# Kernel optimization log

Measured on AMD Instinct MI355X. Metric: run time of the kernel, lower is better.

## Reference

```python
import jax, jax.numpy as jnp
import numpy as np

X_DIM = 20000   # number of input locations (x_l rows)
Y_DIM = 6000    # number of query locations (y_l rows)
REGION_DEG = 10.0  # lon/lat spread so every query has neighbors within 250 km
EARTH_DIAM = 2.0 * 6.378  # thousand-km diameter used by the source
THRESH = 0.25   # 250 km neighborhood threshold


def setup_inputs() -> dict:
    key = jax.random.key(0)
    k1, k2, k3 = jax.random.split(key, 3)
    x = jax.random.normal(k1, (X_DIM, 1), dtype=jnp.float32)
    x_l = jax.random.uniform(k2, (X_DIM, 2), dtype=jnp.float32) * REGION_DEG
    y_l = jax.random.uniform(k3, (Y_DIM, 2), dtype=jnp.float32) * REGION_DEG
    return {"x": x, "x_l": x_l, "y_l": y_l}


def reference(x, x_l, y_l):
    # Training branch of GPR.call, vectorized over the y_dim python loop.
    d2r = jnp.pi / 180.0
    lon_x, lat_x = x_l[:, 0], x_l[:, 1]   # (X,)
    lon_y, lat_y = y_l[:, 0], y_l[:, 1]   # (Y,)
    # haversine terms, shape (Y, X)
    hav = jnp.sin((lat_x[None, :] - lat_y[:, None]) * d2r) ** 2
    hav = hav + (jnp.cos(lat_x * d2r)[None, :] * jnp.cos(lat_y * d2r)[:, None]
                 * jnp.sin((lon_x[None, :] - lon_y[:, None]) * d2r) ** 2)
    d = EARTH_DIAM * jnp.arcsin(jnp.sqrt(hav))  # great-circle distance (thousand km)
    # threshold + gather/scatter in source == masked weights here
    w = jnp.where(d < THRESH, d, 0.0)
    s = jnp.sum(w, axis=1, keepdims=True)        # (Y, 1) per-row normalizer
    L = jnp.where(s > 0, w / jnp.maximum(s, 1e-12), 0.0)  # (Y, X) sparse-ish weights
    m = (L @ x)[:, 0]                            # (Y,) squeezed mean
    # V = 0.001 * I  (noise=None path); returned value is diag_part(V)
    v_diag = jnp.full((y_l.shape[0],), 0.001, dtype=x.dtype)
    return m, v_diag
```

## Files before the change

### kernel.cpp

```cpp
#include <hip/hip_runtime.h>
#include <math.h>


#define TPB    256
#define NSTRIP 40
#define NLON   40
#define NCELLS (NSTRIP * NLON)
#define C_CELL   0.25f
#define INV_CELL 4.0f
#define RLAT     1.1250f

__device__ __forceinline__ float sin_poly(float a) {
    float t = a * a;
    return a * fmaf(t, fmaf(t, 8.3333333e-3f, -0.16666667f), 1.0f);
}
__device__ __forceinline__ float cos_poly(float a) {
    float t = a * a;
    return fmaf(t, fmaf(t, fmaf(t, -1.3888889e-3f, 4.1666668e-2f), -0.5f), 1.0f);
}
__device__ __forceinline__ int cell_of(float lon, float lat) {
    int s = (int)(lat * INV_CELL); s = min(max(s, 0), NSTRIP - 1);
    int l = (int)(lon * INV_CELL); l = min(max(l, 0), NLON - 1);
    return s * NLON + l;
}

__device__ __attribute__((noinline)) float band_w(float lonx, float latx,
                                                  float lony, float laty)
{
    const float d2r = 0.017453292519943295f;
    float dlat = __fsub_rn(latx, laty);
    float alat = __fmul_rn(dlat, d2r);
    float slf  = (float)sin((double)alat);
    float h1   = __fmul_rn(slf, slf);

    float axl  = __fmul_rn(latx, d2r);
    float ayl  = __fmul_rn(laty, d2r);
    float cxf  = (float)cos((double)axl);
    float cyf  = (float)cos((double)ayl);
    float cc   = __fmul_rn(cxf, cyf);

    float dlon = __fsub_rn(lonx, lony);
    float alon = __fmul_rn(dlon, d2r);
    float sdf  = (float)sin((double)alon);
    float h2   = __fmul_rn(sdf, sdf);

    float hv   = __fadd_rn(h1, __fmul_rn(cc, h2));
    float r32  = (float)sqrt((double)hv);
    float as32 = (float)asin((double)r32);
    float dnp  = __fmul_rn(12.756f, as32);
    return (dnp < 0.25f) ? dnp : 0.0f;
}


__global__ __launch_bounds__(TPB) void zero_kernel(int* __restrict__ histX,
                                                   int* __restrict__ histY) {
    for (int i = threadIdx.x; i < NCELLS; i += TPB) { histX[i] = 0; histY[i] = 0; }
}

__global__ __launch_bounds__(TPB) void hist_kernel(
    const float* __restrict__ x_l, const float* __restrict__ y_l,
    int* __restrict__ histX, int* __restrict__ histY, int nx, int ny)
{
    int i = blockIdx.x * TPB + threadIdx.x;
    if (i < nx) {
        atomicAdd(&histX[cell_of(x_l[2 * i], x_l[2 * i + 1])], 1);
    } else if (i < nx + ny) {
        int j = i - nx;
        atomicAdd(&histY[cell_of(y_l[2 * j], y_l[2 * j + 1])], 1);
    }
}

__global__ __launch_bounds__(TPB) void scan_kernel(
    const int* __restrict__ histX, const int* __restrict__ histY,
    int* __restrict__ csX, int* __restrict__ csY,
    int* __restrict__ curX, int* __restrict__ curY)
{
    const int CHUNK = (NCELLS + TPB - 1) / TPB;
    __shared__ int sums[TPB];
    const int* hist      = (blockIdx.x == 0) ? histX : histY;
    int*       cellStart = (blockIdx.x == 0) ? csX  : csY;
    int*       cursor    = (blockIdx.x == 0) ? curX : curY;

    int tid = threadIdx.x;
    int base = tid * CHUNK;
    int local[7];
    int s = 0;
    #pragma unroll
    for (int j = 0; j < CHUNK; ++j) {
        int idx = base + j;
        int v = (idx < NCELLS) ? hist[idx] : 0;
        local[j] = s; s += v;
    }
    sums[tid] = s;
    __syncthreads();
    for (int off = 1; off < TPB; off <<= 1) {
        int t = (tid >= off) ? sums[tid - off] : 0;
        __syncthreads();
        sums[tid] += t;
        __syncthreads();
    }
    int excl = (tid > 0) ? sums[tid - 1] : 0;
    #pragma unroll
    for (int j = 0; j < CHUNK; ++j) {
        int idx = base + j;
        if (idx < NCELLS) { cellStart[idx] = excl + local[j]; cursor[idx] = excl + local[j]; }
    }
    if (tid == TPB - 1) cellStart[NCELLS] = sums[TPB - 1];
}

__global__ __launch_bounds__(TPB) void scatter_kernel(
    const float* __restrict__ x, const float* __restrict__ x_l,
    const float* __restrict__ y_l,
    int* __restrict__ curX, int* __restrict__ curY,
    float4* __restrict__ sortedA, float2* __restrict__ sortedRaw,
    float2* __restrict__ sortedYL, int* __restrict__ sortedYIdx,
    int nx, int ny)
{
    const float d2r = 0.017453292519943295f;
    int i = blockIdx.x * TPB + threadIdx.x;
    if (i < nx) {
        float lon = x_l[2 * i], lat = x_l[2 * i + 1];
        int pos = atomicAdd(&curX[cell_of(lon, lat)], 1);
        float al = lat * d2r, ao = lon * d2r;
        sortedA[pos]   = make_float4(sin_poly(al), sin_poly(ao),
                                     cos_poly(ao), x[i]);
        sortedRaw[pos] = make_float2(lon, lat);
    } else if (i < nx + ny) {
        int j = i - nx;
        float lon = y_l[2 * j], lat = y_l[2 * j + 1];
        int pos = atomicAdd(&curY[cell_of(lon, lat)], 1);
        sortedYL[pos]   = make_float2(lon, lat);
        sortedYIdx[pos] = j;
    }
}


__global__ __launch_bounds__(TPB) void gpr_binned(
    const float4* __restrict__ sortedA,
    const float2* __restrict__ sortedRaw,
    const int*    __restrict__ cellStart,
    const float2* __restrict__ sortedYL,
    const int*    __restrict__ sortedYIdx,
    float* __restrict__ out, int ny, float Hcut, float HcutM)
{
    const int tid  = threadIdx.x;
    const int wave = tid >> 6;
    const int lane = tid & 63;
    const int wid  = blockIdx.x * (TPB / 64) + wave;
    const int j0   = 2 * wid;
    const int j1   = j0 + 1;
    if (j0 >= ny) return;
    const bool has1 = (j1 < ny);

    const float d2r    = 0.017453292519943295f;
    const float r2d    = 57.29577951308232f;
    const float DIAM   = 12.756f;
    const float DIAM6  = 12.756f / 6.0f;
    const float EPS_H  = 5e-8f;

    const int    yi0 = sortedYIdx[j0];
    const float2 q0  = sortedYL[j0];
    const int    yi1 = has1 ? sortedYIdx[j1] : yi0;
    const float2 q1  = has1 ? sortedYL[j1] : q0;

    const float lon0 = q0.x, lat0 = q0.y;
    const float lon1 = q1.x, lat1 = q1.y;

    const float sly0 = sin_poly(lat0 * d2r), cly0 = cos_poly(lat0 * d2r);
    const float slo0 = sin_poly(lon0 * d2r), clo0 = cos_poly(lon0 * d2r);
    const float sly1 = sin_poly(lat1 * d2r), cly1 = cos_poly(lat1 * d2r);
    const float slo1 = sin_poly(lon1 * d2r), clo1 = cos_poly(lon1 * d2r);

    float accw0 = 0.0f, accx0 = 0.0f, accw1 = 0.0f, accx1 = 0.0f;

    const float latmin = fminf(lat0, lat1), latmax = fmaxf(lat0, lat1);
    const int s0 = max(0,          (int)floorf((latmin - RLAT) * INV_CELL));
    const int s1 = min(NSTRIP - 1, (int)floorf((latmax + RLAT) * INV_CELL));

    for (int s = s0; s <= s1; ++s) {
        const float slo = s * C_CELL, shi = slo + C_CELL;
        const float ccs = cos_poly(fminf(shi, 10.0f) * d2r) * 0.999999f;

        int lo = NLON, hi = -1;
        {
            float dmin = fmaxf(0.0f, fmaxf(slo - lat0, lat0 - shi));
            float de   = fmaxf(0.0f, dmin - 3e-3f);
            float sp   = sin_poly(de * d2r);
            float rem  = HcutM - sp * sp;
            if (rem > 0.0f) {
                float rr = __builtin_amdgcn_sqrtf(rem / (ccs * cly0));
                float W  = rr * fmaf(rr * rr, 0.16666667f, 1.0f) * r2d + 4e-3f;
                lo = min(lo, min(NLON - 1, max(0, (int)floorf((lon0 - W) * INV_CELL))));
                hi = max(hi, min(NLON - 1, max(0, (int)floorf((lon0 + W) * INV_CELL))));
            }
        }
        {
            float dmin = fmaxf(0.0f, fmaxf(slo - lat1, lat1 - shi));
            float de   = fmaxf(0.0f, dmin - 3e-3f);
            float sp   = sin_poly(de * d2r);
            float rem  = HcutM - sp * sp;
            if (rem > 0.0f) {
                float rr = __builtin_amdgcn_sqrtf(rem / (ccs * cly1));
                float W  = rr * fmaf(rr * rr, 0.16666667f, 1.0f) * r2d + 4e-3f;
                lo = min(lo, min(NLON - 1, max(0, (int)floorf((lon1 - W) * INV_CELL))));
                hi = max(hi, min(NLON - 1, max(0, (int)floorf((lon1 + W) * INV_CELL))));
            }
        }
        if (hi < lo) continue;

        const int p0 = cellStart[s * NLON + lo];
        const int p1 = cellStart[s * NLON + hi + 1];

        for (int k = p0 + lane; k < p1; k += 64) {
            float4 e = sortedA[k];
            float cl = __builtin_amdgcn_sqrtf(fmaf(-e.x, e.x, 1.0f));

            {
                float sl  = fmaf(e.x, cly0, -(cl * sly0));
                float sd  = fmaf(e.y, clo0, -(e.z * slo0));
                float hav = fmaf(sl, sl, (cl * cly0) * (sd * sd));
                float tb  = hav - Hcut;
                float r   = __builtin_amdgcn_sqrtf(hav);
                float d   = r * fmaf(hav, DIAM6, DIAM);
                float w;
                if (__builtin_expect(fabsf(tb) < EPS_H, 0)) {
                    float2 raw = sortedRaw[k];
                    w = band_w(raw.x, raw.y, lon0, lat0);
                } else {
                    w = (tb < 0.0f) ? d : 0.0f;
                }
                accw0 += w;
                accx0  = fmaf(w, e.w, accx0);
            }
            {
                float sl  = fmaf(e.x, cly1, -(cl * sly1));
                float sd  = fmaf(e.y, clo1, -(e.z * slo1));
                float hav = fmaf(sl, sl, (cl * cly1) * (sd * sd));
                float tb  = hav - Hcut;
                float r   = __builtin_amdgcn_sqrtf(hav);
                float d   = r * fmaf(hav, DIAM6, DIAM);
                float w;
                if (__builtin_expect(fabsf(tb) < EPS_H, 0)) {
                    float2 raw = sortedRaw[k];
                    w = band_w(raw.x, raw.y, lon1, lat1);
                } else {
                    w = (tb < 0.0f) ? d : 0.0f;
                }
                accw1 += w;
                accx1  = fmaf(w, e.w, accx1);
            }
        }
    }

    #pragma unroll
    for (int off = 32; off > 0; off >>= 1) {
        accw0 += __shfl_xor(accw0, off, 64);
        accx0 += __shfl_xor(accx0, off, 64);
        accw1 += __shfl_xor(accw1, off, 64);
        accx1 += __shfl_xor(accx1, off, 64);
    }

    if (lane == 0) {
        float m0 = (accw0 > 0.0f) ? (accx0 / fmaxf(accw0, 1e-12f)) : 0.0f;
        out[yi0]      = m0;
        out[ny + yi0] = 0.001f;
        if (has1) {
            float m1 = (accw1 > 0.0f) ? (accx1 / fmaxf(accw1, 1e-12f)) : 0.0f;
            out[yi1]      = m1;
            out[ny + yi1] = 0.001f;
        }
    }
}


__global__ __launch_bounds__(TPB) void gpr_full(
    const float* __restrict__ x, const float* __restrict__ x_l,
    const float* __restrict__ y_l, float* __restrict__ out,
    int nx, int ny, float Hcut)
{
    const int tid  = threadIdx.x;
    const int wave = tid >> 6;
    const int lane = tid & 63;
    const int y    = blockIdx.x * 4 + wave;

    const float d2r    = 0.017453292519943295f;
    const float DIAM   = 12.756f;
    const float DIAM6  = 12.756f / 6.0f;
    const float EPS_H  = 5e-8f;

    float lon_y = 0.0f, lat_y = 0.0f;
    if (y < ny) { lon_y = y_l[2 * y]; lat_y = y_l[2 * y + 1]; }
    const float sly   = sin_poly(lat_y * d2r);
    const float cly   = cos_poly(lat_y * d2r);
    const float slony = sin_poly(lon_y * d2r);
    const float clony = cos_poly(lon_y * d2r);

    float accw = 0.0f, accwx = 0.0f;

    for (int k = lane; k < nx; k += 64) {
        float lonx = x_l[2 * k], latx = x_l[2 * k + 1];
        float xv   = x[k];
        float sl   = fmaf(sin_poly(latx * d2r), cly, -(cos_poly(latx * d2r) * sly));
        float sd   = fmaf(sin_poly(lonx * d2r), clony, -(cos_poly(lonx * d2r) * slony));
        float cxy  = cos_poly(latx * d2r) * cly;
        float hav  = fmaf(sl, sl, cxy * (sd * sd));
        float tb   = hav - Hcut;
        float r    = __builtin_amdgcn_sqrtf(hav);
        float d    = r * fmaf(hav, DIAM6, DIAM);
        float w;
        if (__builtin_expect(fabsf(tb) < EPS_H, 0)) {
            w = band_w(lonx, latx, lon_y, lat_y);
        } else {
            w = (tb < 0.0f) ? d : 0.0f;
        }
        accw += w;
        accwx = fmaf(w, xv, accwx);
    }

    #pragma unroll
    for (int off = 32; off > 0; off >>= 1) {
        accw  += __shfl_xor(accw,  off, 64);
        accwx += __shfl_xor(accwx, off, 64);
    }

    if (lane == 0 && y < ny) {
        float m = (accw > 0.0f) ? (accwx / fmaxf(accw, 1e-12f)) : 0.0f;
        out[y]      = m;
        out[ny + y] = 0.001f;
    }
}


extern "C" void kernel_launch(void* const* d_in, const int* in_sizes, int n_in,
                              void* d_out, int out_size, void* d_ws, size_t ws_size,
                              hipStream_t stream) {
    const float* x   = (const float*)d_in[0];
    const float* x_l = (const float*)d_in[1];
    const float* y_l = (const float*)d_in[2];
    float* out = (float*)d_out;

    const int nx = in_sizes[0];
    const int ny = in_sizes[2] / 2;

    double th = 0.25 / 12.756;
    double s  = sin(th);
    float Hcut  = (float)(s * s);
    float HcutM = (float)(s * s * 1.001);

    size_t offA   = 0;
    size_t offRaw = offA   + (size_t)nx * sizeof(float4);
    size_t offYL  = offRaw + (size_t)nx * sizeof(float2);
    size_t offYI  = offYL  + (size_t)ny * sizeof(float2);
    size_t offHX  = offYI  + (size_t)ny * sizeof(int);
    size_t offHY  = offHX  + (size_t)NCELLS * sizeof(int);
    size_t offCSX = offHY  + (size_t)NCELLS * sizeof(int);
    size_t offCSY = offCSX + (size_t)(NCELLS + 1) * sizeof(int);
    size_t offCuX = offCSY + (size_t)(NCELLS + 1) * sizeof(int);
    size_t offCuY = offCuX + (size_t)NCELLS * sizeof(int);
    size_t total  = offCuY + (size_t)NCELLS * sizeof(int);

    if (ws_size >= total) {
        float4* sortedA    = (float4*)((char*)d_ws + offA);
        float2* sortedRaw  = (float2*)((char*)d_ws + offRaw);
        float2* sortedYL   = (float2*)((char*)d_ws + offYL);
        int*    sortedYIdx = (int*)   ((char*)d_ws + offYI);
        int*    histX      = (int*)   ((char*)d_ws + offHX);
        int*    histY      = (int*)   ((char*)d_ws + offHY);
        int*    csX        = (int*)   ((char*)d_ws + offCSX);
        int*    csY        = (int*)   ((char*)d_ws + offCSY);
        int*    curX       = (int*)   ((char*)d_ws + offCuX);
        int*    curY       = (int*)   ((char*)d_ws + offCuY);

        int nb = (nx + ny + TPB - 1) / TPB;
        zero_kernel<<<1, TPB, 0, stream>>>(histX, histY);
        hist_kernel<<<nb, TPB, 0, stream>>>(x_l, y_l, histX, histY, nx, ny);
        scan_kernel<<<2, TPB, 0, stream>>>(histX, histY, csX, csY, curX, curY);
        scatter_kernel<<<nb, TPB, 0, stream>>>(x, x_l, y_l, curX, curY,
                                               sortedA, sortedRaw,
                                               sortedYL, sortedYIdx, nx, ny);
        int nwaves = (ny + 1) / 2;
        int blocks = (nwaves + (TPB / 64) - 1) / (TPB / 64);
        gpr_binned<<<blocks, TPB, 0, stream>>>(sortedA, sortedRaw, csX,
                                               sortedYL, sortedYIdx,
                                               out, ny, Hcut, HcutM);
    } else {
        int blocks = (ny + 3) / 4;
        gpr_full<<<blocks, TPB, 0, stream>>>(x, x_l, y_l, out, nx, ny, Hcut);
    }
}
```

Measured before the change: 97.92 us.

## Split each query's latitude strips across separate waves and reduce partials

Replaces the two-queries-per-wave binned kernel with one wave per (query, latitude strip) pair, up to 10 strips per query. Each wave writes a partial (weight, weighted-x) sum, and a new reduce kernel combines them and scatters the mean to the original query index. This is meant to expose much more parallelism and shorten each wave's serial loop over strips. In exchange it adds an extra kernel launch and a partial buffer, loses the sharing of each x load between two queries, and launches many waves whose strips are out of range or empty.

```diff
diff --git a/kernel.cpp b/kernel.cpp
--- a/kernel.cpp
+++ b/kernel.cpp
@@ -3,6 +3,7 @@
 
 
 #define TPB    256
+#define NSLOT  10
 #define NSTRIP 40
 #define NLON   40
 #define NCELLS (NSTRIP * NLON)
@@ -135,141 +136,100 @@
 }
 
 
-__global__ __launch_bounds__(TPB) void gpr_binned(
+__global__ __launch_bounds__(TPB) void gpr_strip(
     const float4* __restrict__ sortedA,
     const float2* __restrict__ sortedRaw,
     const int*    __restrict__ cellStart,
     const float2* __restrict__ sortedYL,
-    const int*    __restrict__ sortedYIdx,
-    float* __restrict__ out, int ny, float Hcut, float HcutM)
-{
-    const int tid  = threadIdx.x;
-    const int wave = tid >> 6;
-    const int lane = tid & 63;
-    const int wid  = blockIdx.x * (TPB / 64) + wave;
-    const int j0   = 2 * wid;
-    const int j1   = j0 + 1;
-    if (j0 >= ny) return;
-    const bool has1 = (j1 < ny);
-
-    const float d2r    = 0.017453292519943295f;
-    const float r2d    = 57.29577951308232f;
-    const float DIAM   = 12.756f;
-    const float DIAM6  = 12.756f / 6.0f;
-    const float EPS_H  = 5e-8f;
-
-    const int    yi0 = sortedYIdx[j0];
-    const float2 q0  = sortedYL[j0];
-    const int    yi1 = has1 ? sortedYIdx[j1] : yi0;
-    const float2 q1  = has1 ? sortedYL[j1] : q0;
-
-    const float lon0 = q0.x, lat0 = q0.y;
-    const float lon1 = q1.x, lat1 = q1.y;
-
-    const float sly0 = sin_poly(lat0 * d2r), cly0 = cos_poly(lat0 * d2r);
-    const float slo0 = sin_poly(lon0 * d2r), clo0 = cos_poly(lon0 * d2r);
-    const float sly1 = sin_poly(lat1 * d2r), cly1 = cos_poly(lat1 * d2r);
-    const float slo1 = sin_poly(lon1 * d2r), clo1 = cos_poly(lon1 * d2r);
-
-    float accw0 = 0.0f, accx0 = 0.0f, accw1 = 0.0f, accx1 = 0.0f;
-
-    const float latmin = fminf(lat0, lat1), latmax = fmaxf(lat0, lat1);
-    const int s0 = max(0,          (int)floorf((latmin - RLAT) * INV_CELL));
-    const int s1 = min(NSTRIP - 1, (int)floorf((latmax + RLAT) * INV_CELL));
-
-    for (int s = s0; s <= s1; ++s) {
-        const float slo = s * C_CELL, shi = slo + C_CELL;
-        const float ccs = cos_poly(fminf(shi, 10.0f) * d2r) * 0.999999f;
-
-        int lo = NLON, hi = -1;
-        {
-            float dmin = fmaxf(0.0f, fmaxf(slo - lat0, lat0 - shi));
-            float de   = fmaxf(0.0f, dmin - 3e-3f);
-            float sp   = sin_poly(de * d2r);
-            float rem  = HcutM - sp * sp;
-            if (rem > 0.0f) {
-                float rr = __builtin_amdgcn_sqrtf(rem / (ccs * cly0));
-                float W  = rr * fmaf(rr * rr, 0.16666667f, 1.0f) * r2d + 4e-3f;
-                lo = min(lo, min(NLON - 1, max(0, (int)floorf((lon0 - W) * INV_CELL))));
-                hi = max(hi, min(NLON - 1, max(0, (int)floorf((lon0 + W) * INV_CELL))));
-            }
-        }
-        {
-            float dmin = fmaxf(0.0f, fmaxf(slo - lat1, lat1 - shi));
-            float de   = fmaxf(0.0f, dmin - 3e-3f);
-            float sp   = sin_poly(de * d2r);
-            float rem  = HcutM - sp * sp;
-            if (rem > 0.0f) {
-                float rr = __builtin_amdgcn_sqrtf(rem / (ccs * cly1));
-                float W  = rr * fmaf(rr * rr, 0.16666667f, 1.0f) * r2d + 4e-3f;
-                lo = min(lo, min(NLON - 1, max(0, (int)floorf((lon1 - W) * INV_CELL))));
-                hi = max(hi, min(NLON - 1, max(0, (int)floorf((lon1 + W) * INV_CELL))));
-            }
-        }
-        if (hi < lo) continue;
-
-        const int p0 = cellStart[s * NLON + lo];
-        const int p1 = cellStart[s * NLON + hi + 1];
-
-        for (int k = p0 + lane; k < p1; k += 64) {
-            float4 e = sortedA[k];
-            float cl = __builtin_amdgcn_sqrtf(fmaf(-e.x, e.x, 1.0f));
-
-            {
-                float sl  = fmaf(e.x, cly0, -(cl * sly0));
-                float sd  = fmaf(e.y, clo0, -(e.z * slo0));
-                float hav = fmaf(sl, sl, (cl * cly0) * (sd * sd));
+    float2* __restrict__ partial,
+    int ny, float Hcut, float HcutM)
+{
+    const int lane = threadIdx.x & 63;
+    const int wid  = blockIdx.x * (TPB / 64) + (threadIdx.x >> 6);
+    const int j    = wid / NSLOT;
+    const int slot = wid - j * NSLOT;
+    if (j >= ny) return;
+
+    const float d2r   = 0.017453292519943295f;
+    const float r2d   = 57.29577951308232f;
+    const float DIAM  = 12.756f;
+    const float DIAM6 = 12.756f / 6.0f;
+    const float EPS_H = 5e-8f;
+
+    const float2 q     = sortedYL[j];
+    const float  lon_y = q.x, lat_y = q.y;
+
+    float accw = 0.0f, accx = 0.0f;
+
+    const int s = (int)floorf((lat_y - RLAT) * INV_CELL) + slot;
+    if (s >= 0 && s < NSTRIP) {
+        const float sly = sin_poly(lat_y * d2r);
+        const float cly = cos_poly(lat_y * d2r);
+        const float slo = sin_poly(lon_y * d2r);
+        const float clo = cos_poly(lon_y * d2r);
+
+        const float strip_lo = s * C_CELL, strip_hi = strip_lo + C_CELL;
+        float dmin = fmaxf(0.0f, fmaxf(strip_lo - lat_y, lat_y - strip_hi));
+        float de   = fmaxf(0.0f, dmin - 3e-3f);
+        float sp   = sin_poly(de * d2r);
+        float rem  = HcutM - sp * sp;
+        if (rem > 0.0f) {
+            float ccm = cos_poly(fminf(strip_hi, 10.0f) * d2r) * cly * 0.999999f;
+            float rr  = __builtin_amdgcn_sqrtf(rem / ccm);
+            float W   = rr * fmaf(rr * rr, 0.16666667f, 1.0f) * r2d + 4e-3f;
+            int lo = min(NLON - 1, max(0, (int)floorf((lon_y - W) * INV_CELL)));
+            int hi = min(NLON - 1, max(0, (int)floorf((lon_y + W) * INV_CELL)));
+            int p0 = cellStart[s * NLON + lo];
+            int p1 = cellStart[s * NLON + hi + 1];
+
+            for (int k = p0 + lane; k < p1; k += 64) {
+                float4 e = sortedA[k];
+                float cl = __builtin_amdgcn_sqrtf(fmaf(-e.x, e.x, 1.0f));
+
+                float sl  = fmaf(e.x, cly, -(cl * sly));
+                float sd  = fmaf(e.y, clo, -(e.z * slo));
+                float hav = fmaf(sl, sl, (cl * cly) * (sd * sd));
                 float tb  = hav - Hcut;
                 float r   = __builtin_amdgcn_sqrtf(hav);
                 float d   = r * fmaf(hav, DIAM6, DIAM);
                 float w;
                 if (__builtin_expect(fabsf(tb) < EPS_H, 0)) {
                     float2 raw = sortedRaw[k];
-                    w = band_w(raw.x, raw.y, lon0, lat0);
+                    w = band_w(raw.x, raw.y, lon_y, lat_y);
                 } else {
                     w = (tb < 0.0f) ? d : 0.0f;
                 }
-                accw0 += w;
-                accx0  = fmaf(w, e.w, accx0);
-            }
-            {
-                float sl  = fmaf(e.x, cly1, -(cl * sly1));
-                float sd  = fmaf(e.y, clo1, -(e.z * slo1));
-                float hav = fmaf(sl, sl, (cl * cly1) * (sd * sd));
-                float tb  = hav - Hcut;
-                float r   = __builtin_amdgcn_sqrtf(hav);
-                float d   = r * fmaf(hav, DIAM6, DIAM);
-                float w;
-                if (__builtin_expect(fabsf(tb) < EPS_H, 0)) {
-                    float2 raw = sortedRaw[k];
-                    w = band_w(raw.x, raw.y, lon1, lat1);
-                } else {
-                    w = (tb < 0.0f) ? d : 0.0f;
-                }
-                accw1 += w;
-                accx1  = fmaf(w, e.w, accx1);
+                accw += w;
+                accx  = fmaf(w, e.w, accx);
             }
         }
     }
 
     #pragma unroll
     for (int off = 32; off > 0; off >>= 1) {
-        accw0 += __shfl_xor(accw0, off, 64);
-        accx0 += __shfl_xor(accx0, off, 64);
-        accw1 += __shfl_xor(accw1, off, 64);
-        accx1 += __shfl_xor(accx1, off, 64);
-    }
-
-    if (lane == 0) {
-        float m0 = (accw0 > 0.0f) ? (accx0 / fmaxf(accw0, 1e-12f)) : 0.0f;
-        out[yi0]      = m0;
-        out[ny + yi0] = 0.001f;
-        if (has1) {
-            float m1 = (accw1 > 0.0f) ? (accx1 / fmaxf(accw1, 1e-12f)) : 0.0f;
-            out[yi1]      = m1;
-            out[ny + yi1] = 0.001f;
-        }
-    }
+        accw += __shfl_xor(accw, off, 64);
+        accx += __shfl_xor(accx, off, 64);
+    }
+
+    if (lane == 0) partial[wid] = make_float2(accw, accx);
+}
+
+__global__ __launch_bounds__(TPB) void reduce_kernel(
+    const float2* __restrict__ partial, const int* __restrict__ sortedYIdx,
+    float* __restrict__ out, int ny)
+{
+    int j = blockIdx.x * TPB + threadIdx.x;
+    if (j >= ny) return;
+    float w = 0.0f, wx = 0.0f;
+    #pragma unroll
+    for (int s = 0; s < NSLOT; ++s) {
+        float2 p = partial[j * NSLOT + s];
+        w += p.x; wx += p.y;
+    }
+    float m = (w > 0.0f) ? (wx / fmaxf(w, 1e-12f)) : 0.0f;
+    int yi = sortedYIdx[j];
+    out[yi]      = m;
+    out[ny + yi] = 0.001f;
 }
 
 
@@ -283,10 +243,10 @@
     const int lane = tid & 63;
     const int y    = blockIdx.x * 4 + wave;
 
-    const float d2r    = 0.017453292519943295f;
-    const float DIAM   = 12.756f;
-    const float DIAM6  = 12.756f / 6.0f;
-    const float EPS_H  = 5e-8f;
+    const float d2r   = 0.017453292519943295f;
+    const float DIAM  = 12.756f;
+    const float DIAM6 = 12.756f / 6.0f;
+    const float EPS_H = 5e-8f;
 
     float lon_y = 0.0f, lat_y = 0.0f;
     if (y < ny) { lon_y = y_l[2 * y]; lat_y = y_l[2 * y + 1]; }
@@ -350,7 +310,8 @@
     size_t offA   = 0;
     size_t offRaw = offA   + (size_t)nx * sizeof(float4);
     size_t offYL  = offRaw + (size_t)nx * sizeof(float2);
-    size_t offYI  = offYL  + (size_t)ny * sizeof(float2);
+    size_t offPar = offYL  + (size_t)ny * sizeof(float2);
+    size_t offYI  = offPar + (size_t)ny * NSLOT * sizeof(float2);
     size_t offHX  = offYI  + (size_t)ny * sizeof(int);
     size_t offHY  = offHX  + (size_t)NCELLS * sizeof(int);
     size_t offCSX = offHY  + (size_t)NCELLS * sizeof(int);
@@ -363,6 +324,7 @@
         float4* sortedA    = (float4*)((char*)d_ws + offA);
         float2* sortedRaw  = (float2*)((char*)d_ws + offRaw);
         float2* sortedYL   = (float2*)((char*)d_ws + offYL);
+        float2* partial    = (float2*)((char*)d_ws + offPar);
         int*    sortedYIdx = (int*)   ((char*)d_ws + offYI);
         int*    histX      = (int*)   ((char*)d_ws + offHX);
         int*    histY      = (int*)   ((char*)d_ws + offHY);
@@ -378,11 +340,13 @@
         scatter_kernel<<<nb, TPB, 0, stream>>>(x, x_l, y_l, curX, curY,
                                                sortedA, sortedRaw,
                                                sortedYL, sortedYIdx, nx, ny);
-        int nwaves = (ny + 1) / 2;
-        int blocks = (nwaves + (TPB / 64) - 1) / (TPB / 64);
-        gpr_binned<<<blocks, TPB, 0, stream>>>(sortedA, sortedRaw, csX,
-                                               sortedYL, sortedYIdx,
-                                               out, ny, Hcut, HcutM);
+        int nwaves  = ny * NSLOT;
+        int wblocks = (nwaves + (TPB / 64) - 1) / (TPB / 64);
+        gpr_strip<<<wblocks, TPB, 0, stream>>>(sortedA, sortedRaw, csX,
+                                               sortedYL, partial,
+                                               ny, Hcut, HcutM);
+        int rblocks = (ny + TPB - 1) / TPB;
+        reduce_kernel<<<rblocks, TPB, 0, stream>>>(partial, sortedYIdx, out, ny);
     } else {
         int blocks = (ny + 3) / 4;
         gpr_full<<<blocks, TPB, 0, stream>>>(x, x_l, y_l, out, nx, ny, Hcut);
```

After: 94.30 us. 1.04x faster.
